# Kernel optimization log

Measured on AMD Instinct MI355X. Metric: run time of the kernel, lower is better.

The kernel has to match this reference:

```python
import jax, jax.numpy as jnp
import numpy as np

IN_FEATURES = 4096
OUT_FEATURES = 4096
N_GROUPS = 32
GROUP_SIZE = IN_FEATURES // N_GROUPS  # 128


def setup_inputs() -> dict:
    key = jax.random.key(0)
    k_x, k_qw, k_s, k_zp, k_b = jax.random.split(key, 5)
    x = jax.random.normal(k_x, (2, 2048, IN_FEATURES), dtype=jnp.float32)
    # 4-bit GPTQ quantized weight values in [0, 16)
    qweight_int = jax.random.randint(k_qw, (IN_FEATURES, OUT_FEATURES), 0, 16, dtype=jnp.int32)
    scales = jax.random.uniform(k_s, (N_GROUPS, OUT_FEATURES), dtype=jnp.float32, minval=0.001, maxval=0.02)
    zero_points = jax.random.randint(k_zp, (N_GROUPS, OUT_FEATURES), 0, 16, dtype=jnp.int32)
    # standard (non-permuted) g_idx: group index per input channel
    g_idx = (jnp.arange(IN_FEATURES, dtype=jnp.int32) // GROUP_SIZE).astype(jnp.int32)
    bias = jax.random.normal(k_b, (OUT_FEATURES,), dtype=jnp.float32)
    return {"x": x, "qweight_int": qweight_int, "scales": scales,
            "zero_points": zero_points, "g_idx": g_idx, "bias": bias}


def reference(x, qweight_int, scales, zero_points, g_idx, bias):
    dtype = x.dtype
    gi = g_idx.astype(jnp.int32)
    # dequantize: W[i, o] = scales[g_idx[i], o] * (q[i, o] - zp[g_idx[i], o])
    qw = qweight_int.astype(dtype)                       # [in, out]
    zp = zero_points.astype(dtype)[gi]                   # [in, out] via gather
    sc = scales.astype(dtype)[gi]                        # [in, out] via gather
    weight = sc * (qw - zp)                              # [in, out]
    out_shape = x.shape[:-1] + (qweight_int.shape[1],)
    x2d = x.reshape(-1, x.shape[-1])                     # [tokens, in]
    out = (x2d @ weight).reshape(out_shape)              # [b, s, out]
    out = out + bias.astype(dtype)
    return out
```

## Files before the change

kernel.cpp:

```cpp
#include <hip/hip_runtime.h>
#include <hip/hip_bf16.h>

typedef int  int4v  __attribute__((ext_vector_type(4)));
typedef int  int16v __attribute__((ext_vector_type(16)));

#define M_DIM 4096
#define N_DIM 4096
#define K_DIM 4096
#define NG 32
#define GS 128

__global__ void prep_kernel(const float* __restrict__ x,
                            signed char* __restrict__ xq,
                            float* __restrict__ sx,
                            const int* __restrict__ qw,
                            const int* __restrict__ zps,
                            signed char* __restrict__ wq) {
    const int tid = threadIdx.x;
    if (blockIdx.x < 4096) {
        __shared__ float red[4];
        __shared__ float inv_s;
        const int m = blockIdx.x;
        const float4* xr = reinterpret_cast<const float4*>(x + (long)m * K_DIM);
        float4 v[4];
        float amax = 0.f;
#pragma unroll
        for (int j = 0; j < 4; ++j) {
            v[j] = xr[tid * 4 + j];
            amax = fmaxf(amax, fmaxf(fmaxf(fabsf(v[j].x), fabsf(v[j].y)),
                                     fmaxf(fabsf(v[j].z), fabsf(v[j].w))));
        }
#pragma unroll
        for (int off = 32; off >= 1; off >>= 1)
            amax = fmaxf(amax, __shfl_xor(amax, off));
        if ((tid & 63) == 0) red[tid >> 6] = amax;
        __syncthreads();
        if (tid == 0) {
            float a = fmaxf(fmaxf(red[0], red[1]), fmaxf(red[2], red[3]));
            sx[m] = a * (1.f / 127.f);
            inv_s = (a > 0.f) ? 127.f / a : 0.f;
        }
        __syncthreads();
        const float inv = inv_s;
        unsigned p[4];
#pragma unroll
        for (int j = 0; j < 4; ++j) {
            int a0 = __float2int_rn(v[j].x * inv);
            int a1 = __float2int_rn(v[j].y * inv);
            int a2 = __float2int_rn(v[j].z * inv);
            int a3 = __float2int_rn(v[j].w * inv);
            p[j] = (a0 & 255) | ((a1 & 255) << 8) | ((a2 & 255) << 16) | ((a3 & 255) << 24);
        }
        *reinterpret_cast<uint4*>(xq + (long)m * K_DIM + tid * 16) =
            make_uint4(p[0], p[1], p[2], p[3]);
        return;
    }
    __shared__ signed char lt[128 * 32];
    const int bx = blockIdx.x - 4096;
    const int n0 = (bx & 127) * 32;
    const int k0 = (bx >> 7) * 128;
    const int g  = bx >> 7;
    const int kl = tid >> 1;
    const int h  = tid & 1;
    int4 qv[4], zv[4];
#pragma unroll
    for (int c = 0; c < 4; ++c) {
        qv[c] = *reinterpret_cast<const int4*>(&qw[(long)(k0 + kl) * N_DIM + n0 + h * 16 + c * 4]);
        zv[c] = *reinterpret_cast<const int4*>(&zps[(long)g * N_DIM + n0 + h * 16 + c * 4]);
    }
    {
        const int swz = ((kl >> 3) & 7) << 2;
        int* ltw = reinterpret_cast<int*>(lt);
#pragma unroll
        for (int c = 0; c < 4; ++c) {
            unsigned d = (unsigned)((qv[c].x - zv[c].x) & 255)
                       | ((unsigned)((qv[c].y - zv[c].y) & 255) << 8)
                       | ((unsigned)((qv[c].z - zv[c].z) & 255) << 16)
                       | ((unsigned)((qv[c].w - zv[c].w) & 255) << 24);
            ltw[(kl * 32 + ((h * 16 + c * 4) ^ swz)) >> 2] = d;
        }
    }
    __syncthreads();
    const int nl = tid >> 3;
    const int kq = tid & 7;
    unsigned acc[4] = {0u, 0u, 0u, 0u};
#pragma unroll
    for (int j = 0; j < 16; ++j) {
        const int kr = kq * 16 + j;
        unsigned by = (unsigned char)lt[kr * 32 + (nl ^ (((kr >> 3) & 7) << 2))];
        acc[j >> 2] |= by << (8 * (j & 3));
    }
    *reinterpret_cast<uint4*>(wq + (long)(n0 + nl) * K_DIM + k0 + kq * 16) =
        make_uint4(acc[0], acc[1], acc[2], acc[3]);
}

#define BM 256
#define BN 256
#define BK 128
#define NT (K_DIM / BK)

__device__ __forceinline__ void async_ld16(const signed char* g, const signed char* l) {
    __builtin_amdgcn_global_load_lds(
        (const __attribute__((address_space(1))) void*)g,
        (__attribute__((address_space(3))) void*)l, 16, 0, 0);
}

__device__ __forceinline__ int16v mf(const int4v a, const int4v b, const int16v c) {
    return __builtin_amdgcn_mfma_i32_32x32x32_i8(a, b, c, 0, 0, 0);
}

__device__ __forceinline__ void read_af(const signed char* Ab, int wm, int mt,
                                        int l32, int half, int4v af[4]) {
    const int m = wm + mt * 32 + l32;
#pragma unroll
    for (int ks = 0; ks < 4; ++ks) {
        const int slot = (2 * ks + half) ^ (m & 7);
        af[ks] = *reinterpret_cast<const int4v*>(&Ab[m * BK + slot * 16]);
    }
}

__device__ __forceinline__ void mfma_phase(const int4v af[4], const int4v bf[2][4],
                                           int16v& c0, int16v& c1) {
    int16v z;
#pragma unroll
    for (int r = 0; r < 16; ++r) z[r] = 0;
    c0 = mf(af[0], bf[0][0], z);
    c1 = mf(af[0], bf[1][0], z);
#pragma unroll
    for (int ks = 1; ks < 4; ++ks) {
        c0 = mf(af[ks], bf[0][ks], c0);
        c1 = mf(af[ks], bf[1][ks], c1);
    }
}

__device__ __forceinline__ void rescale(const int16v& c0, const int16v& c1,
                                        float s0, float s1, float* f0, float* f1) {
#pragma unroll
    for (int r = 0; r < 16; ++r) {
        f0[r] += s0 * (float)c0[r];
        f1[r] += s1 * (float)c1[r];
    }
}

__global__ __launch_bounds__(512, 1) void gemm_kernel(
    const signed char* __restrict__ A,
    const signed char* __restrict__ Bq,
    const float* __restrict__ scales,
    const float* __restrict__ sx,
    const float* __restrict__ bias,
    float* __restrict__ C) {
    __shared__ signed char As[2][BM * BK];
    __shared__ signed char Bs[2][BN * BK];
    const int tid  = threadIdx.x;
    const int wave = tid >> 6;
    const int lane = tid & 63;
    const int half = lane >> 5;
    const int l32  = lane & 31;
    const int wm = (wave >> 2) * 128;
    const int wn = (wave & 3) * 64;

    const int bid = (int)blockIdx.x;
    const int swz = (bid & 7) * 32 + (bid >> 3);
    const int m0 = (swz >> 4) * BM;
    const int n0 = (swz & 15) * BN;

    const int srow  = tid >> 3;
    const int sunit = (tid & 7) ^ (srow & 7);
    const signed char* agp = A  + (long)(m0 + srow) * K_DIM + sunit * 16;
    const signed char* bgp = Bq + (long)(n0 + srow) * K_DIM + sunit * 16;
    const float* sp = scales + n0 + wn + l32;

    float facc[4][2][16];
#pragma unroll
    for (int mt = 0; mt < 4; ++mt)
#pragma unroll
        for (int nt = 0; nt < 2; ++nt)
#pragma unroll
            for (int r = 0; r < 16; ++r) facc[mt][nt][r] = 0.f;

#pragma unroll
    for (int p = 0; p < 4; ++p)
        async_ld16(agp + (long)(p * 64) * K_DIM, As[0] + p * 8192 + wave * 1024);
#pragma unroll
    for (int p = 0; p < 4; ++p)
        async_ld16(bgp + (long)(p * 64) * K_DIM, Bs[0] + p * 8192 + wave * 1024);
    __syncthreads();

    for (int t = 0; t < NT; ++t) {
        const signed char* Ab = As[t & 1];
        const signed char* Bb = Bs[t & 1];
        signed char* Anx = As[(t + 1) & 1];
        signed char* Bnx = Bs[(t + 1) & 1];
        const bool pf = (t + 1 < NT);
        const long kn = (long)(t + 1) * BK;
        int4v bf[2][4];
        int4v af[4];
        int16v c0, c1;

#pragma unroll
        for (int nt = 0; nt < 2; ++nt) {
            const int n = wn + nt * 32 + l32;
#pragma unroll
            for (int ks = 0; ks < 4; ++ks) {
                const int slot = (2 * ks + half) ^ (n & 7);
                bf[nt][ks] = *reinterpret_cast<const int4v*>(&Bb[n * BK + slot * 16]);
            }
        }
        read_af(Ab, wm, 0, l32, half, af);
        if (pf) {
            async_ld16(agp + kn, Anx + wave * 1024);
            async_ld16(agp + (long)64 * K_DIM + kn, Anx + 8192 + wave * 1024);
        }
        const float s0c = sp[(long)t * N_DIM];
        const float s1c = sp[(long)t * N_DIM + 32];
        __builtin_amdgcn_sched_barrier(0);
        __builtin_amdgcn_s_barrier();
        __builtin_amdgcn_sched_barrier(0);
        __builtin_amdgcn_s_setprio(1);
        mfma_phase(af, bf, c0, c1);
        __builtin_amdgcn_s_setprio(0);

        rescale(c0, c1, s0c, s1c, facc[0][0], facc[0][1]);
        read_af(Ab, wm, 1, l32, half, af);
        if (pf) {
            async_ld16(agp + (long)128 * K_DIM + kn, Anx + 16384 + wave * 1024);
            async_ld16(agp + (long)192 * K_DIM + kn, Anx + 24576 + wave * 1024);
        }
        __builtin_amdgcn_sched_barrier(0);
        __builtin_amdgcn_s_barrier();
        __builtin_amdgcn_sched_barrier(0);
        __builtin_amdgcn_s_setprio(1);
        mfma_phase(af, bf, c0, c1);
        __builtin_amdgcn_s_setprio(0);

        rescale(c0, c1, s0c, s1c, facc[1][0], facc[1][1]);
        read_af(Ab, wm, 2, l32, half, af);
        if (pf) {
            async_ld16(bgp + kn, Bnx + wave * 1024);
            async_ld16(bgp + (long)64 * K_DIM + kn, Bnx + 8192 + wave * 1024);
        }
        __builtin_amdgcn_sched_barrier(0);
        __builtin_amdgcn_s_barrier();
        __builtin_amdgcn_sched_barrier(0);
        __builtin_amdgcn_s_setprio(1);
        mfma_phase(af, bf, c0, c1);
        __builtin_amdgcn_s_setprio(0);

        rescale(c0, c1, s0c, s1c, facc[2][0], facc[2][1]);
        read_af(Ab, wm, 3, l32, half, af);
        if (pf) {
            async_ld16(bgp + (long)128 * K_DIM + kn, Bnx + 16384 + wave * 1024);
            async_ld16(bgp + (long)192 * K_DIM + kn, Bnx + 24576 + wave * 1024);
        }
        __builtin_amdgcn_sched_barrier(0);
        __builtin_amdgcn_s_barrier();
        __builtin_amdgcn_sched_barrier(0);
        __builtin_amdgcn_s_setprio(1);
        mfma_phase(af, bf, c0, c1);
        __builtin_amdgcn_s_setprio(0);

        rescale(c0, c1, s0c, s1c, facc[3][0], facc[3][1]);
        __syncthreads();
    }

    float bv[2];
    bv[0] = bias[n0 + wn + l32];
    bv[1] = bias[n0 + wn + 32 + l32];
    const int rowh = half * 4;
#pragma unroll
    for (int mt = 0; mt < 4; ++mt) {
#pragma unroll
        for (int r = 0; r < 16; ++r) {
            const int row = (r & 3) + 8 * (r >> 2) + rowh;
            const int gm  = m0 + wm + mt * 32 + row;
            const float sxm = sx[gm];
            float* crow = C + (long)gm * N_DIM + n0 + wn;
            crow[l32]      = facc[mt][0][r] * sxm + bv[0];
            crow[32 + l32] = facc[mt][1][r] * sxm + bv[1];
        }
    }
}

extern "C" void kernel_launch(void* const* d_in, const int* in_sizes, int n_in,
                              void* d_out, int out_size, void* d_ws, size_t ws_size,
                              hipStream_t stream) {
    const float* x      = (const float*)d_in[0];
    const int*   qw     = (const int*)d_in[1];
    const float* scales = (const float*)d_in[2];
    const int*   zps    = (const int*)d_in[3];
    const float* bias   = (const float*)d_in[5];
    float* out = (float*)d_out;

    signed char* xq = (signed char*)d_ws;
    signed char* wq = (signed char*)d_ws + (size_t)M_DIM * K_DIM;
    float*       sx = (float*)((signed char*)d_ws + 2 * (size_t)M_DIM * K_DIM);

    prep_kernel<<<8192, 256, 0, stream>>>(x, xq, sx, qw, zps, wq);
    gemm_kernel<<<N_DIM / BN * (M_DIM / BM), 512, 0, stream>>>(
        xq, wq, scales, sx, bias, out);
}
```

Before: 272.5 us.

## Use 4-stage 64-wide K pipeline with explicit vmcnt waits and new swizzle

Splits the K loop into 64-byte steps with a 4-buffer LDS ring, prefetching two steps ahead and waiting on vmcnt rather than a full __syncthreads. Each step runs two phases of 8 MFMAs covering paired M tiles, and the integer-accumulator rescale is deferred across barriers. LDS use stays at 128KB and launch_bounds now requests 2 blocks per CU, which likely cannot fit. The aim is deeper overlap of global loads with MFMA work, at the cost of twice as many barriers per unit of K and more register pressure from c[2][2].

After: 786.7 us. 189% more time.

```diff
diff --git a/kernel.cpp b/kernel.cpp
--- a/kernel.cpp
+++ b/kernel.cpp
@@ -96,8 +96,8 @@
 
 #define BM 256
 #define BN 256
-#define BK 128
-#define NT (K_DIM / BK)
+#define KS 64
+#define NSTEP (K_DIM / KS)
 
 __device__ __forceinline__ void async_ld16(const signed char* g, const signed char* l) {
     __builtin_amdgcn_global_load_lds(
@@ -109,48 +109,64 @@
     return __builtin_amdgcn_mfma_i32_32x32x32_i8(a, b, c, 0, 0, 0);
 }
 
-__device__ __forceinline__ void read_af(const signed char* Ab, int wm, int mt,
-                                        int l32, int half, int4v af[4]) {
-    const int m = wm + mt * 32 + l32;
-#pragma unroll
-    for (int ks = 0; ks < 4; ++ks) {
-        const int slot = (2 * ks + half) ^ (m & 7);
-        af[ks] = *reinterpret_cast<const int4v*>(&Ab[m * BK + slot * 16]);
-    }
-}
-
-__device__ __forceinline__ void mfma_phase(const int4v af[4], const int4v bf[2][4],
-                                           int16v& c0, int16v& c1) {
+__device__ __forceinline__ int4v ld_frag(const signed char* buf, int row, int u) {
+    const int phys = u ^ ((row >> 1) & 3);
+    return *reinterpret_cast<const int4v*>(&buf[row * KS + phys * 16]);
+}
+
+__device__ __forceinline__ void wg_barrier() {
+    asm volatile("" ::: "memory");
+    __builtin_amdgcn_s_barrier();
+    asm volatile("" ::: "memory");
+}
+
+template <int P>
+__device__ __forceinline__ void read_af_pair(const signed char* Ab, int wm, int l32,
+                                             int half, int4v af[2][2]) {
+#pragma unroll
+    for (int mtl = 0; mtl < 2; ++mtl) {
+        const int m = wm + (2 * P + mtl) * 32 + l32;
+#pragma unroll
+        for (int ks = 0; ks < 2; ++ks)
+            af[mtl][ks] = ld_frag(Ab, m, 2 * ks + half);
+    }
+}
+
+__device__ __forceinline__ void mfma8(const int4v af[2][2], const int4v bf[2][2],
+                                      int16v c[2][2]) {
     int16v z;
 #pragma unroll
     for (int r = 0; r < 16; ++r) z[r] = 0;
-    c0 = mf(af[0], bf[0][0], z);
-    c1 = mf(af[0], bf[1][0], z);
-#pragma unroll
-    for (int ks = 1; ks < 4; ++ks) {
-        c0 = mf(af[ks], bf[0][ks], c0);
-        c1 = mf(af[ks], bf[1][ks], c1);
-    }
-}
-
-__device__ __forceinline__ void rescale(const int16v& c0, const int16v& c1,
-                                        float s0, float s1, float* f0, float* f1) {
-#pragma unroll
-    for (int r = 0; r < 16; ++r) {
-        f0[r] += s0 * (float)c0[r];
-        f1[r] += s1 * (float)c1[r];
-    }
-}
-
-__global__ __launch_bounds__(512, 1) void gemm_kernel(
+#pragma unroll
+    for (int mtl = 0; mtl < 2; ++mtl)
+#pragma unroll
+        for (int nt = 0; nt < 2; ++nt) {
+            int16v t0 = mf(af[mtl][0], bf[nt][0], z);
+            c[mtl][nt] = mf(af[mtl][1], bf[nt][1], t0);
+        }
+}
+
+template <int P>
+__device__ __forceinline__ void rescale_pair(const int16v c[2][2], float s0, float s1,
+                                             float facc[4][2][16]) {
+#pragma unroll
+    for (int mtl = 0; mtl < 2; ++mtl)
+#pragma unroll
+        for (int r = 0; r < 16; ++r) {
+            facc[2 * P + mtl][0][r] += s0 * (float)c[mtl][0][r];
+            facc[2 * P + mtl][1][r] += s1 * (float)c[mtl][1][r];
+        }
+}
+
+__global__ __launch_bounds__(512, 2) void gemm_kernel(
     const signed char* __restrict__ A,
     const signed char* __restrict__ Bq,
     const float* __restrict__ scales,
     const float* __restrict__ sx,
     const float* __restrict__ bias,
     float* __restrict__ C) {
-    __shared__ signed char As[2][BM * BK];
-    __shared__ signed char Bs[2][BN * BK];
+    __shared__ signed char As[4][BM * KS];
+    __shared__ signed char Bs[4][BN * KS];
     const int tid  = threadIdx.x;
     const int wave = tid >> 6;
     const int lane = tid & 63;
@@ -164,8 +180,8 @@
     const int m0 = (swz >> 4) * BM;
     const int n0 = (swz & 15) * BN;
 
-    const int srow  = tid >> 3;
-    const int sunit = (tid & 7) ^ (srow & 7);
+    const int srow  = tid >> 2;
+    const int sunit = (tid & 3) ^ ((tid >> 3) & 3);
     const signed char* agp = A  + (long)(m0 + srow) * K_DIM + sunit * 16;
     const signed char* bgp = Bq + (long)(n0 + srow) * K_DIM + sunit * 16;
     const float* sp = scales + n0 + wn + l32;
@@ -178,90 +194,68 @@
 #pragma unroll
             for (int r = 0; r < 16; ++r) facc[mt][nt][r] = 0.f;
 
-#pragma unroll
-    for (int p = 0; p < 4; ++p)
-        async_ld16(agp + (long)(p * 64) * K_DIM, As[0] + p * 8192 + wave * 1024);
-#pragma unroll
-    for (int p = 0; p < 4; ++p)
-        async_ld16(bgp + (long)(p * 64) * K_DIM, Bs[0] + p * 8192 + wave * 1024);
-    __syncthreads();
-
-    for (int t = 0; t < NT; ++t) {
-        const signed char* Ab = As[t & 1];
-        const signed char* Bb = Bs[t & 1];
-        signed char* Anx = As[(t + 1) & 1];
-        signed char* Bnx = Bs[(t + 1) & 1];
-        const bool pf = (t + 1 < NT);
-        const long kn = (long)(t + 1) * BK;
-        int4v bf[2][4];
-        int4v af[4];
-        int16v c0, c1;
-
+    async_ld16(agp,                          As[0] + wave * 1024);
+    async_ld16(agp + (long)128 * K_DIM,      As[0] + 8192 + wave * 1024);
+    async_ld16(bgp,                          Bs[0] + wave * 1024);
+    async_ld16(bgp + (long)128 * K_DIM,      Bs[0] + 8192 + wave * 1024);
+    async_ld16(agp + KS,                     As[1] + wave * 1024);
+    async_ld16(agp + (long)128 * K_DIM + KS, As[1] + 8192 + wave * 1024);
+    async_ld16(bgp + KS,                     Bs[1] + wave * 1024);
+    async_ld16(bgp + (long)128 * K_DIM + KS, Bs[1] + 8192 + wave * 1024);
+    asm volatile("s_waitcnt vmcnt(4)" ::: "memory");
+    wg_barrier();
+
+    int4v af[2][2], bf[2][2];
+    int16v c[2][2];
+    float s0c = 0.f, s1c = 0.f;
+
+    for (int t = 0; t < NSTEP; ++t) {
+        const signed char* Ab = As[t & 3];
+        const signed char* Bb = Bs[t & 3];
+        signed char* An = As[(t + 2) & 3];
+        signed char* Bn = Bs[(t + 2) & 3];
+        const bool pf = (t + 2 < NSTEP);
+        const long ko2 = (long)(t + 2) * KS;
+
+        if (t > 0) rescale_pair<1>(c, s0c, s1c, facc);
+        if ((t & 1) == 0) {
+            s0c = sp[(long)(t >> 1) * N_DIM];
+            s1c = sp[(long)(t >> 1) * N_DIM + 32];
+        }
+        read_af_pair<0>(Ab, wm, l32, half, af);
 #pragma unroll
         for (int nt = 0; nt < 2; ++nt) {
             const int n = wn + nt * 32 + l32;
 #pragma unroll
-            for (int ks = 0; ks < 4; ++ks) {
-                const int slot = (2 * ks + half) ^ (n & 7);
-                bf[nt][ks] = *reinterpret_cast<const int4v*>(&Bb[n * BK + slot * 16]);
-            }
-        }
-        read_af(Ab, wm, 0, l32, half, af);
+            for (int ks = 0; ks < 2; ++ks)
+                bf[nt][ks] = ld_frag(Bb, n, 2 * ks + half);
+        }
         if (pf) {
-            async_ld16(agp + kn, Anx + wave * 1024);
-            async_ld16(agp + (long)64 * K_DIM + kn, Anx + 8192 + wave * 1024);
-        }
-        const float s0c = sp[(long)t * N_DIM];
-        const float s1c = sp[(long)t * N_DIM + 32];
-        __builtin_amdgcn_sched_barrier(0);
-        __builtin_amdgcn_s_barrier();
-        __builtin_amdgcn_sched_barrier(0);
+            async_ld16(agp + ko2,                     An + wave * 1024);
+            async_ld16(agp + (long)128 * K_DIM + ko2, An + 8192 + wave * 1024);
+        }
+        wg_barrier();
         __builtin_amdgcn_s_setprio(1);
-        mfma_phase(af, bf, c0, c1);
+        mfma8(af, bf, c);
         __builtin_amdgcn_s_setprio(0);
-
-        rescale(c0, c1, s0c, s1c, facc[0][0], facc[0][1]);
-        read_af(Ab, wm, 1, l32, half, af);
+        wg_barrier();
+
+        rescale_pair<0>(c, s0c, s1c, facc);
+        read_af_pair<1>(Ab, wm, l32, half, af);
         if (pf) {
-            async_ld16(agp + (long)128 * K_DIM + kn, Anx + 16384 + wave * 1024);
-            async_ld16(agp + (long)192 * K_DIM + kn, Anx + 24576 + wave * 1024);
-        }
-        __builtin_amdgcn_sched_barrier(0);
-        __builtin_amdgcn_s_barrier();
-        __builtin_amdgcn_sched_barrier(0);
+            async_ld16(bgp + ko2,                     Bn + wave * 1024);
+            async_ld16(bgp + (long)128 * K_DIM + ko2, Bn + 8192 + wave * 1024);
+            asm volatile("s_waitcnt vmcnt(4)" ::: "memory");
+        } else {
+            asm volatile("s_waitcnt vmcnt(0)" ::: "memory");
+        }
+        wg_barrier();
         __builtin_amdgcn_s_setprio(1);
-        mfma_phase(af, bf, c0, c1);
+        mfma8(af, bf, c);
         __builtin_amdgcn_s_setprio(0);
-
-        rescale(c0, c1, s0c, s1c, facc[1][0], facc[1][1]);
-        read_af(Ab, wm, 2, l32, half, af);
-        if (pf) {
-            async_ld16(bgp + kn, Bnx + wave * 1024);
-            async_ld16(bgp + (long)64 * K_DIM + kn, Bnx + 8192 + wave * 1024);
-        }
-        __builtin_amdgcn_sched_barrier(0);
-        __builtin_amdgcn_s_barrier();
-        __builtin_amdgcn_sched_barrier(0);
-        __builtin_amdgcn_s_setprio(1);
-        mfma_phase(af, bf, c0, c1);
-        __builtin_amdgcn_s_setprio(0);
-
-        rescale(c0, c1, s0c, s1c, facc[2][0], facc[2][1]);
-        read_af(Ab, wm, 3, l32, half, af);
-        if (pf) {
-            async_ld16(bgp + (long)128 * K_DIM + kn, Bnx + 16384 + wave * 1024);
-            async_ld16(bgp + (long)192 * K_DIM + kn, Bnx + 24576 + wave * 1024);
-        }
-        __builtin_amdgcn_sched_barrier(0);
-        __builtin_amdgcn_s_barrier();
-        __builtin_amdgcn_sched_barrier(0);
-        __builtin_amdgcn_s_setprio(1);
-        mfma_phase(af, bf, c0, c1);
-        __builtin_amdgcn_s_setprio(0);
-
-        rescale(c0, c1, s0c, s1c, facc[3][0], facc[3][1]);
-        __syncthreads();
-    }
+        wg_barrier();
+    }
+    rescale_pair<1>(c, s0c, s1c, facc);
 
     float bv[2];
     bv[0] = bias[n0 + wn + l32];
```
